# Kernel optimization log

Hardware: AMD Instinct MI355X
Metric: run time of the kernel (lower is better)

## Reference

```python
import jax, jax.numpy as jnp
import numpy as np

N = 50000      # num nodes
E = 800000     # num edges (no self loops; added in reference like add_remaining_self_loops)
D = 64         # input_dim
H = 128        # hidden_dim
O = 32         # output_dim
EPS = 1.0      # epsilon (privacy)
ALPHA = 0.5
DELTA = 1.0


def setup_inputs() -> dict:
    key = jax.random.key(0)
    ks = jax.random.split(key, 8)
    x = jax.random.normal(ks[0], (N, D), dtype=jnp.float32)
    row = jax.random.randint(ks[1], (E,), 0, N, dtype=jnp.int32)
    off = jax.random.randint(ks[2], (E,), 1, N, dtype=jnp.int32)
    col = (row + off) % N  # guarantees row != col (no pre-existing self loops)
    edge_index = jnp.stack([row, col], axis=0)
    priv_mask = jax.random.bernoulli(ks[3], 0.5, (N,))
    W1 = jax.random.normal(ks[4], (D, H), dtype=jnp.float32) * (1.0 / np.sqrt(D))
    b1 = jnp.zeros((H,), dtype=jnp.float32)
    W2 = jax.random.normal(ks[5], (H, O), dtype=jnp.float32) * (1.0 / np.sqrt(H))
    b2 = jnp.zeros((O,), dtype=jnp.float32)
    return {"x": x, "edge_index": edge_index, "priv_mask": priv_mask,
            "W1": W1, "b1": b1, "W2": W2, "b2": b2}


def _gcn_norm(edge_index, num_nodes, dtype):
    # add_remaining_self_loops + symmetric normalization deg^-1/2[row]*deg^-1/2[col]
    loops = jnp.arange(num_nodes, dtype=edge_index.dtype)
    row = jnp.concatenate([edge_index[0], loops])
    col = jnp.concatenate([edge_index[1], loops])
    deg = jax.ops.segment_sum(jnp.ones(row.shape[0], dtype=dtype), row,
                              num_segments=num_nodes)
    dis = deg ** -0.5  # deg >= 1 thanks to self loops
    norm = dis[row] * dis[col]  # [E+N]
    return row, col, norm


def reference(x, edge_index, priv_mask, W1, b1, W2, b2):
    row, col, norm = _gcn_norm(edge_index, N, x.dtype)
    exp_eps = float(np.exp(EPS))

    # ---- conv1 (GConvDP with per-node bool priv_mask) ----
    x_j = x[row]                                   # [E+N, D] gather
    p = priv_mask[row].astype(x.dtype)[:, None]    # [E+N, 1]
    transformed = ((exp_eps + 1.0) * x_j - 1.0) * (DELTA / (exp_eps - 1.0)) + ALPHA
    msg = norm[:, None] * (p * transformed + (1.0 - p) * x_j)
    h = jax.ops.segment_sum(msg, col, num_segments=N)  # scatter-add aggregate

    h = jax.nn.relu(h @ W1 + b1)
    # F.dropout skipped: reference is deterministic (eval mode)

    # ---- conv2 (called with priv_mask=False, a Python scalar) ----
    # Literal torch semantics: p_j = False -> False*(...) = 0, ~False = -1,
    # so msg = norm * (-x_j).
    msg2 = -norm[:, None] * h[row]                 # [E+N, H]
    h2 = jax.ops.segment_sum(msg2, col, num_segments=N)

    return h2 @ W2 + b2
```

## Files before the change

kernel.cpp:

```cpp
#include <hip/hip_runtime.h>
#include <math.h>

#define C1 2.163953413738653f
#define C0 -0.081976706869326f


typedef __attribute__((ext_vector_type(8))) short bf16x8;
typedef __attribute__((ext_vector_type(4))) float f32x4;

static __device__ __forceinline__ unsigned short f2bf(float f) {
    unsigned b = __float_as_uint(f);
    return (unsigned short)((b + 0x7FFFu + ((b >> 16) & 1u)) >> 16);
}
static __device__ __forceinline__ float bf2f(unsigned short u) {
    return __uint_as_float((unsigned)u << 16);
}
static __device__ __forceinline__ float bfl(unsigned u) { return __uint_as_float(u << 16); }
static __device__ __forceinline__ float bfh(unsigned u) { return __uint_as_float(u & 0xFFFF0000u); }

__global__ __launch_bounds__(1024) void k_hist2(const int* __restrict__ row,
                                                const int* __restrict__ col, int E, int chunk,
                                                int* __restrict__ hist,
                                                const float* __restrict__ W1,
                                                const float* __restrict__ W2,
                                                unsigned short* __restrict__ W1b,
                                                unsigned short* __restrict__ W2b) {
    __shared__ int hc[256], hr[256];
    int t = threadIdx.x, b = blockIdx.x;
    if (t < 256) { hc[t] = 0; hr[t] = 0; }
    __syncthreads();
    int lo = b * chunk, hi = min(E, lo + chunk);
    int base = lo + t * 4;
    for (; base + 3 < hi; base += 4096) {
        int4 r4 = *(const int4*)&row[base];
        int4 c4 = *(const int4*)&col[base];
        atomicAdd(&hc[c4.x >> 8], 1); atomicAdd(&hc[c4.y >> 8], 1);
        atomicAdd(&hc[c4.z >> 8], 1); atomicAdd(&hc[c4.w >> 8], 1);
        atomicAdd(&hr[r4.x >> 8], 1); atomicAdd(&hr[r4.y >> 8], 1);
        atomicAdd(&hr[r4.z >> 8], 1); atomicAdd(&hr[r4.w >> 8], 1);
    }
    for (; base < hi; ++base) {
        atomicAdd(&hc[col[base] >> 8], 1);
        atomicAdd(&hr[row[base] >> 8], 1);
    }
    __syncthreads();
    if (t < 256) {
        hist[t * 256 + b] = hc[t];
        hist[65536 + t * 256 + b] = hr[t];
    }
    if (b == 0) {
        for (int i = t; i < 8192; i += 1024) {
            int j = i & 7, l2 = (i >> 3) & 63, kt = (i >> 9) & 1, nt = i >> 10;
            int k = kt * 32 + (l2 >> 4) * 8 + j, n = nt * 16 + (l2 & 15);
            W1b[i] = f2bf(W1[k * 128 + n]);
        }
    } else if (b == 1) {
        for (int i = t; i < 4096; i += 1024) {
            int j = i & 7, l2 = (i >> 3) & 63, kt = (i >> 9) & 3, nt = i >> 11;
            int k = kt * 32 + (l2 >> 4) * 8 + j, n = nt * 16 + (l2 & 15);
            W2b[i] = f2bf(W2[k * 32 + n]);
        }
    }
}

__global__ void k_scan_a(const int* __restrict__ cnt, int* __restrict__ excl,
                         int* __restrict__ bsum, int n) {
    __shared__ int s[256];
    int idx = blockIdx.x * 256 + threadIdx.x;
    int v = (idx < n) ? cnt[idx] : 0;
    s[threadIdx.x] = v;
    __syncthreads();
    for (int off = 1; off < 256; off <<= 1) {
        int t = (threadIdx.x >= off) ? s[threadIdx.x - off] : 0;
        __syncthreads();
        s[threadIdx.x] += t;
        __syncthreads();
    }
    if (idx < n) excl[idx] = s[threadIdx.x] - v;
    if (threadIdx.x == 255) bsum[blockIdx.x] = s[255];
}

__global__ __launch_bounds__(1024) void k_part(const int* __restrict__ row,
                                               const int* __restrict__ col, int E, int chunk,
                                               const int* __restrict__ excl,
                                               const int* __restrict__ bsum,
                                               unsigned* __restrict__ cbuf,
                                               unsigned char* __restrict__ rbuf) {
    __shared__ int sc[512];
    __shared__ int offc[256], offr[256];
    int t = threadIdx.x, b = blockIdx.x;
    if (t < 512) sc[t] = bsum[t];
    __syncthreads();
    int half = t >> 8, d = t & 255;
    for (int off = 1; off < 256; off <<= 1) {
        int u = (t < 512 && d >= off) ? sc[half * 256 + d - off] : 0;
        __syncthreads();
        if (t < 512) sc[t] += u;
        __syncthreads();
    }
    if (t < 256) offc[t] = sc[t] - bsum[t] + excl[t * 256 + b];
    else if (t < 512) offr[d] = sc[t] - bsum[t] + excl[65536 + d * 256 + b];
    __syncthreads();
    int lo = b * chunk, hi = min(E, lo + chunk);
    int base = lo + t * 4;
    for (; base + 3 < hi; base += 4096) {
        int4 r4 = *(const int4*)&row[base];
        int4 c4 = *(const int4*)&col[base];
        int p0 = atomicAdd(&offc[c4.x >> 8], 1);
        cbuf[p0] = ((unsigned)c4.x << 16) | (unsigned)r4.x;
        int p1 = atomicAdd(&offc[c4.y >> 8], 1);
        cbuf[p1] = ((unsigned)c4.y << 16) | (unsigned)r4.y;
        int p2 = atomicAdd(&offc[c4.z >> 8], 1);
        cbuf[p2] = ((unsigned)c4.z << 16) | (unsigned)r4.z;
        int p3 = atomicAdd(&offc[c4.w >> 8], 1);
        cbuf[p3] = ((unsigned)c4.w << 16) | (unsigned)r4.w;
        int q0 = atomicAdd(&offr[r4.x >> 8], 1); rbuf[q0] = (unsigned char)r4.x;
        int q1 = atomicAdd(&offr[r4.y >> 8], 1); rbuf[q1] = (unsigned char)r4.y;
        int q2 = atomicAdd(&offr[r4.z >> 8], 1); rbuf[q2] = (unsigned char)r4.z;
        int q3 = atomicAdd(&offr[r4.w >> 8], 1); rbuf[q3] = (unsigned char)r4.w;
    }
    for (; base < hi; ++base) {
        int r = row[base], c = col[base];
        int pc = atomicAdd(&offc[c >> 8], 1);
        cbuf[pc] = ((unsigned)c << 16) | (unsigned)r;
        int pr = atomicAdd(&offr[r >> 8], 1);
        rbuf[pr] = (unsigned char)r;
    }
}

__global__ __launch_bounds__(256) void k_build(const unsigned char* __restrict__ rbuf,
                                               const unsigned* __restrict__ cbuf,
                                               const int* __restrict__ bsum,
                                               const int* __restrict__ priv,
                                               const float* __restrict__ x, int N, int E, int nbk,
                                               float* __restrict__ dis,
                                               unsigned short* __restrict__ xt,
                                               int* __restrict__ cntC, int* __restrict__ colStart,
                                               unsigned short* __restrict__ eSrc) {
    __shared__ int s1[256], s2[256], s3[256];
    int t = threadIdx.x;
    if ((int)blockIdx.x < nbk) {
        int b = blockIdx.x;
        s1[t] = (t < b) ? bsum[256 + t] : 0;
        __syncthreads();
        for (int off = 128; off > 0; off >>= 1) {
            if (t < off) s1[t] += s1[t + off];
            __syncthreads();
        }
        int rs = s1[0];
        int re = rs + bsum[256 + b];
        __syncthreads();
        s1[t] = 0;
        __syncthreads();
        for (int i = rs + t; i < re; i += 256) atomicAdd(&s1[rbuf[i]], 1);
        __syncthreads();
        int node = b * 256 + t;
        float dv = rsqrtf((float)(s1[t] + 1));
        if (node < N) {
            dis[node] = dv;
            s2[t] = __float_as_int(dv);
            s3[t] = priv[node];
        } else { s2[t] = 0; s3[t] = 0; }
        __syncthreads();
        int base = b * 256;
        for (int i = t; i < 256 * 16; i += 256) {
            int ln = i >> 4;
            int n2 = base + ln;
            if (n2 >= N) continue;
            float d2 = __int_as_float(s2[ln]);
            int p = s3[ln];
            float4 v = ((const float4*)x)[(size_t)n2 * 16 + (i & 15)];
            float4 tr;
            tr.x = p ? fmaf(C1, v.x, C0) : v.x;
            tr.y = p ? fmaf(C1, v.y, C0) : v.y;
            tr.z = p ? fmaf(C1, v.z, C0) : v.z;
            tr.w = p ? fmaf(C1, v.w, C0) : v.w;
            ushort4 o;
            o.x = f2bf(d2 * tr.x); o.y = f2bf(d2 * tr.y);
            o.z = f2bf(d2 * tr.z); o.w = f2bf(d2 * tr.w);
            ((ushort4*)xt)[(size_t)n2 * 16 + (i & 15)] = o;
        }
    } else {
        int b = blockIdx.x - nbk;
        s1[t] = (t < b) ? bsum[t] : 0;
        __syncthreads();
        for (int off = 128; off > 0; off >>= 1) {
            if (t < off) s1[t] += s1[t + off];
            __syncthreads();
        }
        int cs = s1[0];
        int ce = cs + bsum[b];
        __syncthreads();
        s1[t] = 0; s3[t] = 0;
        __syncthreads();
        for (int i = cs + t; i < ce; i += 256) atomicAdd(&s1[(cbuf[i] >> 16) & 255], 1);
        __syncthreads();
        int v = s1[t];
        s2[t] = v;
        __syncthreads();
        for (int off = 1; off < 256; off <<= 1) {
            int u = (t >= off) ? s2[t - off] : 0;
            __syncthreads();
            s2[t] += u;
            __syncthreads();
        }
        int excl = s2[t] - v;
        int c = b * 256 + t;
        if (c < N) { cntC[c] = v; colStart[c] = cs + excl; }
        __syncthreads();
        s2[t] = excl;
        __syncthreads();
        for (int i = cs + t; i < ce; i += 256) {
            unsigned e = cbuf[i];
            int d = (e >> 16) & 255;
            int pos = cs + s2[d] + atomicAdd(&s3[d], 1);
            eSrc[pos] = (unsigned short)(e & 0xFFFFu);
        }
    }
}

__global__ __launch_bounds__(256) void k_gather1(const unsigned short* __restrict__ xt,
                                                 const unsigned short* __restrict__ eSrc,
                                                 const int* __restrict__ colStart,
                                                 const int* __restrict__ cntC,
                                                 const float* __restrict__ dis,
                                                 unsigned short* __restrict__ agg1b, int N) {
    int t = blockIdx.x * blockDim.x + threadIdx.x;
    int c = t >> 4, j = t & 15;
    if (c >= N) return;
    const uint2* x64 = (const uint2*)xt;
    uint2 u = x64[(size_t)c * 16 + j];
    float s0 = bfl(u.x), s1 = bfh(u.x), s2 = bfl(u.y), s3 = bfh(u.y);
    int start = colStart[c], cnt = cntC[c];
    for (int base = 0; base < cnt; base += 16) {
        int m = min(cnt - base, 16);
        int ids = (j < m) ? (int)eSrc[start + base + j] : 0;
        int k = 0;
        for (; k + 8 <= m; k += 8) {
            int r0 = __shfl(ids, k, 16),     r1 = __shfl(ids, k + 1, 16);
            int r2 = __shfl(ids, k + 2, 16), r3 = __shfl(ids, k + 3, 16);
            int r4 = __shfl(ids, k + 4, 16), r5 = __shfl(ids, k + 5, 16);
            int r6 = __shfl(ids, k + 6, 16), r7 = __shfl(ids, k + 7, 16);
            uint2 u0 = x64[(size_t)r0 * 16 + j];
            uint2 u1 = x64[(size_t)r1 * 16 + j];
            uint2 u2 = x64[(size_t)r2 * 16 + j];
            uint2 u3 = x64[(size_t)r3 * 16 + j];
            uint2 u4 = x64[(size_t)r4 * 16 + j];
            uint2 u5 = x64[(size_t)r5 * 16 + j];
            uint2 u6 = x64[(size_t)r6 * 16 + j];
            uint2 u7 = x64[(size_t)r7 * 16 + j];
            s0 += bfl(u0.x); s1 += bfh(u0.x); s2 += bfl(u0.y); s3 += bfh(u0.y);
            s0 += bfl(u1.x); s1 += bfh(u1.x); s2 += bfl(u1.y); s3 += bfh(u1.y);
            s0 += bfl(u2.x); s1 += bfh(u2.x); s2 += bfl(u2.y); s3 += bfh(u2.y);
            s0 += bfl(u3.x); s1 += bfh(u3.x); s2 += bfl(u3.y); s3 += bfh(u3.y);
            s0 += bfl(u4.x); s1 += bfh(u4.x); s2 += bfl(u4.y); s3 += bfh(u4.y);
            s0 += bfl(u5.x); s1 += bfh(u5.x); s2 += bfl(u5.y); s3 += bfh(u5.y);
            s0 += bfl(u6.x); s1 += bfh(u6.x); s2 += bfl(u6.y); s3 += bfh(u6.y);
            s0 += bfl(u7.x); s1 += bfh(u7.x); s2 += bfl(u7.y); s3 += bfh(u7.y);
        }
        for (; k + 4 <= m; k += 4) {
            int r0 = __shfl(ids, k, 16),     r1 = __shfl(ids, k + 1, 16);
            int r2 = __shfl(ids, k + 2, 16), r3 = __shfl(ids, k + 3, 16);
            uint2 u0 = x64[(size_t)r0 * 16 + j];
            uint2 u1 = x64[(size_t)r1 * 16 + j];
            uint2 u2 = x64[(size_t)r2 * 16 + j];
            uint2 u3 = x64[(size_t)r3 * 16 + j];
            s0 += bfl(u0.x); s1 += bfh(u0.x); s2 += bfl(u0.y); s3 += bfh(u0.y);
            s0 += bfl(u1.x); s1 += bfh(u1.x); s2 += bfl(u1.y); s3 += bfh(u1.y);
            s0 += bfl(u2.x); s1 += bfh(u2.x); s2 += bfl(u2.y); s3 += bfh(u2.y);
            s0 += bfl(u3.x); s1 += bfh(u3.x); s2 += bfl(u3.y); s3 += bfh(u3.y);
        }
        for (; k < m; ++k) {
            int r = __shfl(ids, k, 16);
            uint2 uu = x64[(size_t)r * 16 + j];
            s0 += bfl(uu.x); s1 += bfh(uu.x); s2 += bfl(uu.y); s3 += bfh(uu.y);
        }
    }
    float dv = dis[c];
    uint2 o;
    o.x = ((unsigned)f2bf(dv * s1) << 16) | (unsigned)f2bf(dv * s0);
    o.y = ((unsigned)f2bf(dv * s3) << 16) | (unsigned)f2bf(dv * s2);
    ((uint2*)agg1b)[(size_t)c * 16 + j] = o;
}

__global__ __launch_bounds__(256) void k_mlp_mfma(const unsigned short* __restrict__ agg1b,
                                                  const unsigned short* __restrict__ W1b,
                                                  const float* __restrict__ b1,
                                                  const unsigned short* __restrict__ W2b,
                                                  const float* __restrict__ dis,
                                                  unsigned short* __restrict__ hps, int N) {
    __shared__ unsigned short hidA[4][16 * 136];
    const int t = threadIdx.x;
    const int w = t >> 6, l = t & 63;
    const int q = l >> 4, lm = l & 15;
    const int rowbase = blockIdx.x * 64 + w * 16;

    bf16x8 a0, a1;
    {
        int node = rowbase + lm;
        if (node >= N) node = N - 1;
        const bf16x8* pa = (const bf16x8*)(agg1b + (size_t)node * 64);
        a0 = pa[q];
        a1 = pa[4 + q];
    }
    float dvals[4];
    #pragma unroll
    for (int r = 0; r < 4; ++r) {
        int node = rowbase + q * 4 + r;
        dvals[r] = (node < N) ? dis[node] : 0.f;
    }

    const bf16x8* w1f = (const bf16x8*)W1b;
    #pragma unroll
    for (int nt = 0; nt < 8; ++nt) {
        float bv = b1[nt * 16 + lm];
        f32x4 acc = {bv, bv, bv, bv};
        acc = __builtin_amdgcn_mfma_f32_16x16x32_bf16(a0, w1f[(nt * 2 + 0) * 64 + l], acc, 0, 0, 0);
        acc = __builtin_amdgcn_mfma_f32_16x16x32_bf16(a1, w1f[(nt * 2 + 1) * 64 + l], acc, 0, 0, 0);
        #pragma unroll
        for (int r = 0; r < 4; ++r)
            hidA[w][(q * 4 + r) * 136 + nt * 16 + lm] = f2bf(fmaxf(acc[r], 0.f));
    }
    __syncthreads();

    bf16x8 ha[4];
    #pragma unroll
    for (int kt = 0; kt < 4; ++kt)
        ha[kt] = *(const bf16x8*)&hidA[w][lm * 136 + kt * 32 + q * 8];

    const bf16x8* w2f = (const bf16x8*)W2b;
    #pragma unroll
    for (int nt = 0; nt < 2; ++nt) {
        f32x4 acc = {0.f, 0.f, 0.f, 0.f};
        #pragma unroll
        for (int kt = 0; kt < 4; ++kt)
            acc = __builtin_amdgcn_mfma_f32_16x16x32_bf16(ha[kt], w2f[(nt * 4 + kt) * 64 + l], acc, 0, 0, 0);
        #pragma unroll
        for (int r = 0; r < 4; ++r) {
            int node = rowbase + q * 4 + r;
            if (node < N)
                hps[(size_t)node * 32 + nt * 16 + lm] = f2bf(acc[r] * dvals[r]);
        }
    }
}

__global__ __launch_bounds__(256) void k_gather2(const unsigned short* __restrict__ hps,
                                                 const unsigned short* __restrict__ eSrc,
                                                 const int* __restrict__ colStart,
                                                 const int* __restrict__ cntC,
                                                 const float* __restrict__ dis,
                                                 const float* __restrict__ b2,
                                                 float* __restrict__ out, int N) {
    int t = blockIdx.x * blockDim.x + threadIdx.x;
    int c = t >> 3, j = t & 7;
    if (c >= N) return;
    const uint2* h64 = (const uint2*)hps;
    uint2 u = h64[(size_t)c * 8 + j];
    float s0 = bfl(u.x), s1 = bfh(u.x), s2 = bfl(u.y), s3 = bfh(u.y);
    int start = colStart[c], cnt = cntC[c];
    for (int base = 0; base < cnt; base += 8) {
        int m = min(cnt - base, 8);
        int ids = (j < m) ? (int)eSrc[start + base + j] : 0;
        int k = 0;
        for (; k + 8 <= m; k += 8) {
            int r0 = __shfl(ids, k, 8),     r1 = __shfl(ids, k + 1, 8);
            int r2 = __shfl(ids, k + 2, 8), r3 = __shfl(ids, k + 3, 8);
            int r4 = __shfl(ids, k + 4, 8), r5 = __shfl(ids, k + 5, 8);
            int r6 = __shfl(ids, k + 6, 8), r7 = __shfl(ids, k + 7, 8);
            uint2 u0 = h64[(size_t)r0 * 8 + j];
            uint2 u1 = h64[(size_t)r1 * 8 + j];
            uint2 u2 = h64[(size_t)r2 * 8 + j];
            uint2 u3 = h64[(size_t)r3 * 8 + j];
            uint2 u4 = h64[(size_t)r4 * 8 + j];
            uint2 u5 = h64[(size_t)r5 * 8 + j];
            uint2 u6 = h64[(size_t)r6 * 8 + j];
            uint2 u7 = h64[(size_t)r7 * 8 + j];
            s0 += bfl(u0.x); s1 += bfh(u0.x); s2 += bfl(u0.y); s3 += bfh(u0.y);
            s0 += bfl(u1.x); s1 += bfh(u1.x); s2 += bfl(u1.y); s3 += bfh(u1.y);
            s0 += bfl(u2.x); s1 += bfh(u2.x); s2 += bfl(u2.y); s3 += bfh(u2.y);
            s0 += bfl(u3.x); s1 += bfh(u3.x); s2 += bfl(u3.y); s3 += bfh(u3.y);
            s0 += bfl(u4.x); s1 += bfh(u4.x); s2 += bfl(u4.y); s3 += bfh(u4.y);
            s0 += bfl(u5.x); s1 += bfh(u5.x); s2 += bfl(u5.y); s3 += bfh(u5.y);
            s0 += bfl(u6.x); s1 += bfh(u6.x); s2 += bfl(u6.y); s3 += bfh(u6.y);
            s0 += bfl(u7.x); s1 += bfh(u7.x); s2 += bfl(u7.y); s3 += bfh(u7.y);
        }
        for (; k + 4 <= m; k += 4) {
            int r0 = __shfl(ids, k, 8),     r1 = __shfl(ids, k + 1, 8);
            int r2 = __shfl(ids, k + 2, 8), r3 = __shfl(ids, k + 3, 8);
            uint2 u0 = h64[(size_t)r0 * 8 + j];
            uint2 u1 = h64[(size_t)r1 * 8 + j];
            uint2 u2 = h64[(size_t)r2 * 8 + j];
            uint2 u3 = h64[(size_t)r3 * 8 + j];
            s0 += bfl(u0.x); s1 += bfh(u0.x); s2 += bfl(u0.y); s3 += bfh(u0.y);
            s0 += bfl(u1.x); s1 += bfh(u1.x); s2 += bfl(u1.y); s3 += bfh(u1.y);
            s0 += bfl(u2.x); s1 += bfh(u2.x); s2 += bfl(u2.y); s3 += bfh(u2.y);
            s0 += bfl(u3.x); s1 += bfh(u3.x); s2 += bfl(u3.y); s3 += bfh(u3.y);
        }
        for (; k < m; ++k) {
            int r = __shfl(ids, k, 8);
            uint2 uu = h64[(size_t)r * 8 + j];
            s0 += bfl(uu.x); s1 += bfh(uu.x); s2 += bfl(uu.y); s3 += bfh(uu.y);
        }
    }
    float dv = dis[c];
    float4 bb = ((const float4*)b2)[j];
    float4 o;
    o.x = bb.x - dv * s0;
    o.y = bb.y - dv * s1;
    o.z = bb.z - dv * s2;
    o.w = bb.w - dv * s3;
    ((float4*)out)[(size_t)c * 8 + j] = o;
}

extern "C" void kernel_launch(void* const* d_in, const int* in_sizes, int n_in,
                              void* d_out, int out_size, void* d_ws, size_t ws_size,
                              hipStream_t stream) {
    const float* x    = (const float*)d_in[0];
    const int*   ei   = (const int*)d_in[1];
    const int*   priv = (const int*)d_in[2];
    const float* W1   = (const float*)d_in[3];
    const float* b1   = (const float*)d_in[4];
    const float* W2   = (const float*)d_in[5];
    const float* b2   = (const float*)d_in[6];
    float* out = (float*)d_out;

    const int N = in_sizes[2];
    const int E = in_sizes[1] / 2;
    const int* row = ei;
    const int* col = ei + E;

    char* ws = (char*)d_ws;
    size_t off = 0;
    auto take = [&](size_t bytes) { char* p = ws + off; off = (off + bytes + 255) & ~(size_t)255; return p; };
    int*            hist     = (int*)           take((size_t)131072 * 4);
    int*            excl     = (int*)           take((size_t)131072 * 4);
    int*            bsum     = (int*)           take(512 * 4);
    unsigned short* W1b      = (unsigned short*)take((size_t)8192 * 2);
    unsigned short* W2b      = (unsigned short*)take((size_t)4096 * 2);
    unsigned*       cbuf     = (unsigned*)      take((size_t)E * 4);
    unsigned char*  rbuf     = (unsigned char*) take((size_t)E);
    float*          dis      = (float*)         take((size_t)N * 4);
    int*            cntC     = (int*)           take((size_t)N * 4);
    int*            colStart = (int*)           take((size_t)N * 4);
    unsigned short* eSrc     = (unsigned short*)take((size_t)E * 2);
    unsigned short* xt       = (unsigned short*)take((size_t)N * 64 * 2);
    unsigned short* agg1b    = (unsigned short*)take((size_t)N * 64 * 2);
    unsigned short* hps      = (unsigned short*)take((size_t)N * 32 * 2);
    (void)ws_size;

    const int chunk = (((E + 255) / 256) + 3) & ~3;
    const int nbk = (N + 255) / 256;

    k_hist2   <<<256, 1024, 0, stream>>>(row, col, E, chunk, hist, W1, W2, W1b, W2b);
    k_scan_a  <<<512, 256, 0, stream>>>(hist, excl, bsum, 131072);
    k_part    <<<256, 1024, 0, stream>>>(row, col, E, chunk, excl, bsum, cbuf, rbuf);
    k_build   <<<2 * nbk, 256, 0, stream>>>(rbuf, cbuf, bsum, priv, x, N, E, nbk,
                                            dis, xt, cntC, colStart, eSrc);
    k_gather1 <<<((size_t)N * 16 + 255) / 256, 256, 0, stream>>>(xt, eSrc, colStart, cntC, dis, agg1b, N);
    k_mlp_mfma<<<(N + 63) / 64, 256, 0, stream>>>(agg1b, W1b, b1, W2b, dis, hps, N);
    k_gather2 <<<((size_t)N * 8 + 255) / 256, 256, 0, stream>>>(hps, eSrc, colStart, cntC, dis, b2, out, N);
}
```

Before: 145.2 us.

## Assign a full wavefront per node in both gather kernels with zero-padded sentinel rows

The two gather kernels now give each destination node a whole 64-lane wavefront instead of 16 or 8 lanes. Sub-groups of lanes fetch different neighbours at the same time and are combined with xor-shuffle reductions. Out-of-range neighbour slots point to a new zero row appended to xt and hps, which k_hist2 clears, so the tail loops need no per-lane branching. This raises memory-level parallelism for the average degree of about 16. The cost is four times more threads, idle lanes on low-degree nodes, and extra shuffle and reduction work.

```diff
diff --git a/kernel.cpp b/kernel.cpp
--- a/kernel.cpp
+++ b/kernel.cpp
@@ -24,7 +24,9 @@
                                                 const float* __restrict__ W1,
                                                 const float* __restrict__ W2,
                                                 unsigned short* __restrict__ W1b,
-                                                unsigned short* __restrict__ W2b) {
+                                                unsigned short* __restrict__ W2b,
+                                                unsigned short* __restrict__ xt,
+                                                unsigned short* __restrict__ hps, int N) {
     __shared__ int hc[256], hr[256];
     int t = threadIdx.x, b = blockIdx.x;
     if (t < 256) { hc[t] = 0; hr[t] = 0; }
@@ -60,6 +62,9 @@
             int k = kt * 32 + (l2 >> 4) * 8 + j, n = nt * 16 + (l2 & 15);
             W2b[i] = f2bf(W2[k * 32 + n]);
         }
+    } else if (b == 2) {
+        if (t < 64) xt[(size_t)N * 64 + t] = 0;
+        else if (t < 96) hps[(size_t)N * 32 + (t - 64)] = 0;
     }
 }
 
@@ -225,42 +230,23 @@
                                                  const int* __restrict__ cntC,
                                                  const float* __restrict__ dis,
                                                  unsigned short* __restrict__ agg1b, int N) {
-    int t = blockIdx.x * blockDim.x + threadIdx.x;
-    int c = t >> 4, j = t & 15;
+    int c = (blockIdx.x * blockDim.x + threadIdx.x) >> 6;
     if (c >= N) return;
+    int lane = threadIdx.x & 63;
+    int j = lane & 15;
+    int g = lane >> 4;
     const uint2* x64 = (const uint2*)xt;
-    uint2 u = x64[(size_t)c * 16 + j];
-    float s0 = bfl(u.x), s1 = bfh(u.x), s2 = bfl(u.y), s3 = bfh(u.y);
+    float s0 = 0.f, s1 = 0.f, s2 = 0.f, s3 = 0.f;
     int start = colStart[c], cnt = cntC[c];
-    for (int base = 0; base < cnt; base += 16) {
-        int m = min(cnt - base, 16);
-        int ids = (j < m) ? (int)eSrc[start + base + j] : 0;
+    for (int base = 0; base < cnt; base += 64) {
+        int m = min(cnt - base, 64);
+        int ids = (lane < m) ? (int)eSrc[start + base + lane] : N;
         int k = 0;
-        for (; k + 8 <= m; k += 8) {
-            int r0 = __shfl(ids, k, 16),     r1 = __shfl(ids, k + 1, 16);
-            int r2 = __shfl(ids, k + 2, 16), r3 = __shfl(ids, k + 3, 16);
-            int r4 = __shfl(ids, k + 4, 16), r5 = __shfl(ids, k + 5, 16);
-            int r6 = __shfl(ids, k + 6, 16), r7 = __shfl(ids, k + 7, 16);
-            uint2 u0 = x64[(size_t)r0 * 16 + j];
-            uint2 u1 = x64[(size_t)r1 * 16 + j];
-            uint2 u2 = x64[(size_t)r2 * 16 + j];
-            uint2 u3 = x64[(size_t)r3 * 16 + j];
-            uint2 u4 = x64[(size_t)r4 * 16 + j];
-            uint2 u5 = x64[(size_t)r5 * 16 + j];
-            uint2 u6 = x64[(size_t)r6 * 16 + j];
-            uint2 u7 = x64[(size_t)r7 * 16 + j];
-            s0 += bfl(u0.x); s1 += bfh(u0.x); s2 += bfl(u0.y); s3 += bfh(u0.y);
-            s0 += bfl(u1.x); s1 += bfh(u1.x); s2 += bfl(u1.y); s3 += bfh(u1.y);
-            s0 += bfl(u2.x); s1 += bfh(u2.x); s2 += bfl(u2.y); s3 += bfh(u2.y);
-            s0 += bfl(u3.x); s1 += bfh(u3.x); s2 += bfl(u3.y); s3 += bfh(u3.y);
-            s0 += bfl(u4.x); s1 += bfh(u4.x); s2 += bfl(u4.y); s3 += bfh(u4.y);
-            s0 += bfl(u5.x); s1 += bfh(u5.x); s2 += bfl(u5.y); s3 += bfh(u5.y);
-            s0 += bfl(u6.x); s1 += bfh(u6.x); s2 += bfl(u6.y); s3 += bfh(u6.y);
-            s0 += bfl(u7.x); s1 += bfh(u7.x); s2 += bfl(u7.y); s3 += bfh(u7.y);
-        }
-        for (; k + 4 <= m; k += 4) {
-            int r0 = __shfl(ids, k, 16),     r1 = __shfl(ids, k + 1, 16);
-            int r2 = __shfl(ids, k + 2, 16), r3 = __shfl(ids, k + 3, 16);
+        for (; k + 16 <= m; k += 16) {
+            int r0 = __shfl(ids, k + g, 64);
+            int r1 = __shfl(ids, k + 4 + g, 64);
+            int r2 = __shfl(ids, k + 8 + g, 64);
+            int r3 = __shfl(ids, k + 12 + g, 64);
             uint2 u0 = x64[(size_t)r0 * 16 + j];
             uint2 u1 = x64[(size_t)r1 * 16 + j];
             uint2 u2 = x64[(size_t)r2 * 16 + j];
@@ -270,17 +256,25 @@
             s0 += bfl(u2.x); s1 += bfh(u2.x); s2 += bfl(u2.y); s3 += bfh(u2.y);
             s0 += bfl(u3.x); s1 += bfh(u3.x); s2 += bfl(u3.y); s3 += bfh(u3.y);
         }
-        for (; k < m; ++k) {
-            int r = __shfl(ids, k, 16);
-            uint2 uu = x64[(size_t)r * 16 + j];
-            s0 += bfl(uu.x); s1 += bfh(uu.x); s2 += bfl(uu.y); s3 += bfh(uu.y);
-        }
-    }
-    float dv = dis[c];
-    uint2 o;
-    o.x = ((unsigned)f2bf(dv * s1) << 16) | (unsigned)f2bf(dv * s0);
-    o.y = ((unsigned)f2bf(dv * s3) << 16) | (unsigned)f2bf(dv * s2);
-    ((uint2*)agg1b)[(size_t)c * 16 + j] = o;
+        for (; k < m; k += 4) {
+            int r = __shfl(ids, k + g, 64);
+            uint2 u = x64[(size_t)r * 16 + j];
+            s0 += bfl(u.x); s1 += bfh(u.x); s2 += bfl(u.y); s3 += bfh(u.y);
+        }
+    }
+    s0 += __shfl_xor(s0, 32, 64); s1 += __shfl_xor(s1, 32, 64);
+    s2 += __shfl_xor(s2, 32, 64); s3 += __shfl_xor(s3, 32, 64);
+    s0 += __shfl_xor(s0, 16, 64); s1 += __shfl_xor(s1, 16, 64);
+    s2 += __shfl_xor(s2, 16, 64); s3 += __shfl_xor(s3, 16, 64);
+    if (g == 0) {
+        uint2 u = x64[(size_t)c * 16 + j];
+        s0 += bfl(u.x); s1 += bfh(u.x); s2 += bfl(u.y); s3 += bfh(u.y);
+        float dv = dis[c];
+        uint2 o;
+        o.x = ((unsigned)f2bf(dv * s1) << 16) | (unsigned)f2bf(dv * s0);
+        o.y = ((unsigned)f2bf(dv * s3) << 16) | (unsigned)f2bf(dv * s2);
+        ((uint2*)agg1b)[(size_t)c * 16 + j] = o;
+    }
 }
 
 __global__ __launch_bounds__(256) void k_mlp_mfma(const unsigned short* __restrict__ agg1b,
@@ -351,65 +345,50 @@
                                                  const float* __restrict__ dis,
                                                  const float* __restrict__ b2,
                                                  float* __restrict__ out, int N) {
-    int t = blockIdx.x * blockDim.x + threadIdx.x;
-    int c = t >> 3, j = t & 7;
+    int c = (blockIdx.x * blockDim.x + threadIdx.x) >> 6;
     if (c >= N) return;
+    int lane = threadIdx.x & 63;
+    int j = lane & 7;
+    int g = lane >> 3;
     const uint2* h64 = (const uint2*)hps;
-    uint2 u = h64[(size_t)c * 8 + j];
-    float s0 = bfl(u.x), s1 = bfh(u.x), s2 = bfl(u.y), s3 = bfh(u.y);
+    float s0 = 0.f, s1 = 0.f, s2 = 0.f, s3 = 0.f;
     int start = colStart[c], cnt = cntC[c];
-    for (int base = 0; base < cnt; base += 8) {
-        int m = min(cnt - base, 8);
-        int ids = (j < m) ? (int)eSrc[start + base + j] : 0;
+    for (int base = 0; base < cnt; base += 64) {
+        int m = min(cnt - base, 64);
+        int ids = (lane < m) ? (int)eSrc[start + base + lane] : N;
         int k = 0;
-        for (; k + 8 <= m; k += 8) {
-            int r0 = __shfl(ids, k, 8),     r1 = __shfl(ids, k + 1, 8);
-            int r2 = __shfl(ids, k + 2, 8), r3 = __shfl(ids, k + 3, 8);
-            int r4 = __shfl(ids, k + 4, 8), r5 = __shfl(ids, k + 5, 8);
-            int r6 = __shfl(ids, k + 6, 8), r7 = __shfl(ids, k + 7, 8);
+        for (; k + 16 <= m; k += 16) {
+            int r0 = __shfl(ids, k + g, 64);
+            int r1 = __shfl(ids, k + 8 + g, 64);
             uint2 u0 = h64[(size_t)r0 * 8 + j];
             uint2 u1 = h64[(size_t)r1 * 8 + j];
-            uint2 u2 = h64[(size_t)r2 * 8 + j];
-            uint2 u3 = h64[(size_t)r3 * 8 + j];
-            uint2 u4 = h64[(size_t)r4 * 8 + j];
-            uint2 u5 = h64[(size_t)r5 * 8 + j];
-            uint2 u6 = h64[(size_t)r6 * 8 + j];
-            uint2 u7 = h64[(size_t)r7 * 8 + j];
             s0 += bfl(u0.x); s1 += bfh(u0.x); s2 += bfl(u0.y); s3 += bfh(u0.y);
             s0 += bfl(u1.x); s1 += bfh(u1.x); s2 += bfl(u1.y); s3 += bfh(u1.y);
-            s0 += bfl(u2.x); s1 += bfh(u2.x); s2 += bfl(u2.y); s3 += bfh(u2.y);
-            s0 += bfl(u3.x); s1 += bfh(u3.x); s2 += bfl(u3.y); s3 += bfh(u3.y);
-            s0 += bfl(u4.x); s1 += bfh(u4.x); s2 += bfl(u4.y); s3 += bfh(u4.y);
-            s0 += bfl(u5.x); s1 += bfh(u5.x); s2 += bfl(u5.y); s3 += bfh(u5.y);
-            s0 += bfl(u6.x); s1 += bfh(u6.x); s2 += bfl(u6.y); s3 += bfh(u6.y);
-            s0 += bfl(u7.x); s1 += bfh(u7.x); s2 += bfl(u7.y); s3 += bfh(u7.y);
-        }
-        for (; k + 4 <= m; k += 4) {
-            int r0 = __shfl(ids, k, 8),     r1 = __shfl(ids, k + 1, 8);
-            int r2 = __shfl(ids, k + 2, 8), r3 = __shfl(ids, k + 3, 8);
-            uint2 u0 = h64[(size_t)r0 * 8 + j];
-            uint2 u1 = h64[(size_t)r1 * 8 + j];
-            uint2 u2 = h64[(size_t)r2 * 8 + j];
-            uint2 u3 = h64[(size_t)r3 * 8 + j];
-            s0 += bfl(u0.x); s1 += bfh(u0.x); s2 += bfl(u0.y); s3 += bfh(u0.y);
-            s0 += bfl(u1.x); s1 += bfh(u1.x); s2 += bfl(u1.y); s3 += bfh(u1.y);
-            s0 += bfl(u2.x); s1 += bfh(u2.x); s2 += bfl(u2.y); s3 += bfh(u2.y);
-            s0 += bfl(u3.x); s1 += bfh(u3.x); s2 += bfl(u3.y); s3 += bfh(u3.y);
-        }
-        for (; k < m; ++k) {
-            int r = __shfl(ids, k, 8);
-            uint2 uu = h64[(size_t)r * 8 + j];
-            s0 += bfl(uu.x); s1 += bfh(uu.x); s2 += bfl(uu.y); s3 += bfh(uu.y);
-        }
-    }
-    float dv = dis[c];
-    float4 bb = ((const float4*)b2)[j];
-    float4 o;
-    o.x = bb.x - dv * s0;
-    o.y = bb.y - dv * s1;
-    o.z = bb.z - dv * s2;
-    o.w = bb.w - dv * s3;
-    ((float4*)out)[(size_t)c * 8 + j] = o;
+        }
+        for (; k < m; k += 8) {
+            int r = __shfl(ids, k + g, 64);
+            uint2 u = h64[(size_t)r * 8 + j];
+            s0 += bfl(u.x); s1 += bfh(u.x); s2 += bfl(u.y); s3 += bfh(u.y);
+        }
+    }
+    s0 += __shfl_xor(s0, 32, 64); s1 += __shfl_xor(s1, 32, 64);
+    s2 += __shfl_xor(s2, 32, 64); s3 += __shfl_xor(s3, 32, 64);
+    s0 += __shfl_xor(s0, 16, 64); s1 += __shfl_xor(s1, 16, 64);
+    s2 += __shfl_xor(s2, 16, 64); s3 += __shfl_xor(s3, 16, 64);
+    s0 += __shfl_xor(s0, 8, 64);  s1 += __shfl_xor(s1, 8, 64);
+    s2 += __shfl_xor(s2, 8, 64);  s3 += __shfl_xor(s3, 8, 64);
+    if (g == 0) {
+        uint2 u = h64[(size_t)c * 8 + j];
+        s0 += bfl(u.x); s1 += bfh(u.x); s2 += bfl(u.y); s3 += bfh(u.y);
+        float dv = dis[c];
+        float4 bb = ((const float4*)b2)[j];
+        float4 o;
+        o.x = bb.x - dv * s0;
+        o.y = bb.y - dv * s1;
+        o.z = bb.z - dv * s2;
+        o.w = bb.w - dv * s3;
+        ((float4*)out)[(size_t)c * 8 + j] = o;
+    }
 }
 
 extern "C" void kernel_launch(void* const* d_in, const int* in_sizes, int n_in,
@@ -443,20 +422,20 @@
     int*            cntC     = (int*)           take((size_t)N * 4);
     int*            colStart = (int*)           take((size_t)N * 4);
     unsigned short* eSrc     = (unsigned short*)take((size_t)E * 2);
-    unsigned short* xt       = (unsigned short*)take((size_t)N * 64 * 2);
+    unsigned short* xt       = (unsigned short*)take((size_t)(N + 1) * 64 * 2);
     unsigned short* agg1b    = (unsigned short*)take((size_t)N * 64 * 2);
-    unsigned short* hps      = (unsigned short*)take((size_t)N * 32 * 2);
+    unsigned short* hps      = (unsigned short*)take((size_t)(N + 1) * 32 * 2);
     (void)ws_size;
 
     const int chunk = (((E + 255) / 256) + 3) & ~3;
     const int nbk = (N + 255) / 256;
 
-    k_hist2   <<<256, 1024, 0, stream>>>(row, col, E, chunk, hist, W1, W2, W1b, W2b);
+    k_hist2   <<<256, 1024, 0, stream>>>(row, col, E, chunk, hist, W1, W2, W1b, W2b, xt, hps, N);
     k_scan_a  <<<512, 256, 0, stream>>>(hist, excl, bsum, 131072);
     k_part    <<<256, 1024, 0, stream>>>(row, col, E, chunk, excl, bsum, cbuf, rbuf);
     k_build   <<<2 * nbk, 256, 0, stream>>>(rbuf, cbuf, bsum, priv, x, N, E, nbk,
                                             dis, xt, cntC, colStart, eSrc);
-    k_gather1 <<<((size_t)N * 16 + 255) / 256, 256, 0, stream>>>(xt, eSrc, colStart, cntC, dis, agg1b, N);
+    k_gather1 <<<((size_t)N * 64 + 255) / 256, 256, 0, stream>>>(xt, eSrc, colStart, cntC, dis, agg1b, N);
     k_mlp_mfma<<<(N + 63) / 64, 256, 0, stream>>>(agg1b, W1b, b1, W2b, dis, hps, N);
-    k_gather2 <<<((size_t)N * 8 + 255) / 256, 256, 0, stream>>>(hps, eSrc, colStart, cntC, dis, b2, out, N);
-}
+    k_gather2 <<<((size_t)N * 64 + 255) / 256, 256, 0, stream>>>(hps, eSrc, colStart, cntC, dis, b2, out, N);
+}
```

Result: slower. 159.2 us (+9.6%).

## Fuse first-layer gather into MLP kernel via shared-memory aggregate tile

Applied to the files above, without the earlier changes.

Merges the layer-1 neighbor gather with the MFMA MLP kernel. Each 256-thread block gathers 64 nodes (16 lanes per node, four passes) into a padded LDS tile, then runs the W1/W2 MFMA stages from LDS. This drops the agg1b global write and read-back and one kernel launch. In exchange the gather runs with fewer blocks, each doing four sequential node passes, which may reduce memory-level parallelism and latency hiding.

```diff
diff --git a/kernel.cpp b/kernel.cpp
--- a/kernel.cpp
+++ b/kernel.cpp
@@ -219,90 +219,87 @@
     }
 }
 
-__global__ __launch_bounds__(256) void k_gather1(const unsigned short* __restrict__ xt,
-                                                 const unsigned short* __restrict__ eSrc,
-                                                 const int* __restrict__ colStart,
-                                                 const int* __restrict__ cntC,
-                                                 const float* __restrict__ dis,
-                                                 unsigned short* __restrict__ agg1b, int N) {
-    int t = blockIdx.x * blockDim.x + threadIdx.x;
-    int c = t >> 4, j = t & 15;
-    if (c >= N) return;
-    const uint2* x64 = (const uint2*)xt;
-    uint2 u = x64[(size_t)c * 16 + j];
-    float s0 = bfl(u.x), s1 = bfh(u.x), s2 = bfl(u.y), s3 = bfh(u.y);
-    int start = colStart[c], cnt = cntC[c];
-    for (int base = 0; base < cnt; base += 16) {
-        int m = min(cnt - base, 16);
-        int ids = (j < m) ? (int)eSrc[start + base + j] : 0;
-        int k = 0;
-        for (; k + 8 <= m; k += 8) {
-            int r0 = __shfl(ids, k, 16),     r1 = __shfl(ids, k + 1, 16);
-            int r2 = __shfl(ids, k + 2, 16), r3 = __shfl(ids, k + 3, 16);
-            int r4 = __shfl(ids, k + 4, 16), r5 = __shfl(ids, k + 5, 16);
-            int r6 = __shfl(ids, k + 6, 16), r7 = __shfl(ids, k + 7, 16);
-            uint2 u0 = x64[(size_t)r0 * 16 + j];
-            uint2 u1 = x64[(size_t)r1 * 16 + j];
-            uint2 u2 = x64[(size_t)r2 * 16 + j];
-            uint2 u3 = x64[(size_t)r3 * 16 + j];
-            uint2 u4 = x64[(size_t)r4 * 16 + j];
-            uint2 u5 = x64[(size_t)r5 * 16 + j];
-            uint2 u6 = x64[(size_t)r6 * 16 + j];
-            uint2 u7 = x64[(size_t)r7 * 16 + j];
-            s0 += bfl(u0.x); s1 += bfh(u0.x); s2 += bfl(u0.y); s3 += bfh(u0.y);
-            s0 += bfl(u1.x); s1 += bfh(u1.x); s2 += bfl(u1.y); s3 += bfh(u1.y);
-            s0 += bfl(u2.x); s1 += bfh(u2.x); s2 += bfl(u2.y); s3 += bfh(u2.y);
-            s0 += bfl(u3.x); s1 += bfh(u3.x); s2 += bfl(u3.y); s3 += bfh(u3.y);
-            s0 += bfl(u4.x); s1 += bfh(u4.x); s2 += bfl(u4.y); s3 += bfh(u4.y);
-            s0 += bfl(u5.x); s1 += bfh(u5.x); s2 += bfl(u5.y); s3 += bfh(u5.y);
-            s0 += bfl(u6.x); s1 += bfh(u6.x); s2 += bfl(u6.y); s3 += bfh(u6.y);
-            s0 += bfl(u7.x); s1 += bfh(u7.x); s2 += bfl(u7.y); s3 += bfh(u7.y);
-        }
-        for (; k + 4 <= m; k += 4) {
-            int r0 = __shfl(ids, k, 16),     r1 = __shfl(ids, k + 1, 16);
-            int r2 = __shfl(ids, k + 2, 16), r3 = __shfl(ids, k + 3, 16);
-            uint2 u0 = x64[(size_t)r0 * 16 + j];
-            uint2 u1 = x64[(size_t)r1 * 16 + j];
-            uint2 u2 = x64[(size_t)r2 * 16 + j];
-            uint2 u3 = x64[(size_t)r3 * 16 + j];
-            s0 += bfl(u0.x); s1 += bfh(u0.x); s2 += bfl(u0.y); s3 += bfh(u0.y);
-            s0 += bfl(u1.x); s1 += bfh(u1.x); s2 += bfl(u1.y); s3 += bfh(u1.y);
-            s0 += bfl(u2.x); s1 += bfh(u2.x); s2 += bfl(u2.y); s3 += bfh(u2.y);
-            s0 += bfl(u3.x); s1 += bfh(u3.x); s2 += bfl(u3.y); s3 += bfh(u3.y);
-        }
-        for (; k < m; ++k) {
-            int r = __shfl(ids, k, 16);
-            uint2 uu = x64[(size_t)r * 16 + j];
-            s0 += bfl(uu.x); s1 += bfh(uu.x); s2 += bfl(uu.y); s3 += bfh(uu.y);
-        }
-    }
-    float dv = dis[c];
-    uint2 o;
-    o.x = ((unsigned)f2bf(dv * s1) << 16) | (unsigned)f2bf(dv * s0);
-    o.y = ((unsigned)f2bf(dv * s3) << 16) | (unsigned)f2bf(dv * s2);
-    ((uint2*)agg1b)[(size_t)c * 16 + j] = o;
-}
-
-__global__ __launch_bounds__(256) void k_mlp_mfma(const unsigned short* __restrict__ agg1b,
-                                                  const unsigned short* __restrict__ W1b,
-                                                  const float* __restrict__ b1,
-                                                  const unsigned short* __restrict__ W2b,
-                                                  const float* __restrict__ dis,
-                                                  unsigned short* __restrict__ hps, int N) {
+__global__ __launch_bounds__(256) void k_gmlp(const unsigned short* __restrict__ xt,
+                                              const unsigned short* __restrict__ eSrc,
+                                              const int* __restrict__ colStart,
+                                              const int* __restrict__ cntC,
+                                              const float* __restrict__ dis,
+                                              const unsigned short* __restrict__ W1b,
+                                              const float* __restrict__ b1,
+                                              const unsigned short* __restrict__ W2b,
+                                              unsigned short* __restrict__ hps, int N) {
+    __shared__ unsigned short agg[64 * 72];
     __shared__ unsigned short hidA[4][16 * 136];
     const int t = threadIdx.x;
+    const int grp = t >> 4, j = t & 15;
+    const uint2* x64 = (const uint2*)xt;
+
+    for (int it = 0; it < 4; ++it) {
+        int ln = grp + it * 16;
+        int c = blockIdx.x * 64 + ln;
+        uint2 o; o.x = 0u; o.y = 0u;
+        if (c < N) {
+            uint2 u = x64[(size_t)c * 16 + j];
+            float s0 = bfl(u.x), s1 = bfh(u.x), s2 = bfl(u.y), s3 = bfh(u.y);
+            int start = colStart[c], cnt = cntC[c];
+            for (int base = 0; base < cnt; base += 16) {
+                int m = min(cnt - base, 16);
+                int ids = (j < m) ? (int)eSrc[start + base + j] : 0;
+                int k = 0;
+                for (; k + 8 <= m; k += 8) {
+                    int r0 = __shfl(ids, k, 16),     r1 = __shfl(ids, k + 1, 16);
+                    int r2 = __shfl(ids, k + 2, 16), r3 = __shfl(ids, k + 3, 16);
+                    int r4 = __shfl(ids, k + 4, 16), r5 = __shfl(ids, k + 5, 16);
+                    int r6 = __shfl(ids, k + 6, 16), r7 = __shfl(ids, k + 7, 16);
+                    uint2 u0 = x64[(size_t)r0 * 16 + j];
+                    uint2 u1 = x64[(size_t)r1 * 16 + j];
+                    uint2 u2 = x64[(size_t)r2 * 16 + j];
+                    uint2 u3 = x64[(size_t)r3 * 16 + j];
+                    uint2 u4 = x64[(size_t)r4 * 16 + j];
+                    uint2 u5 = x64[(size_t)r5 * 16 + j];
+                    uint2 u6 = x64[(size_t)r6 * 16 + j];
+                    uint2 u7 = x64[(size_t)r7 * 16 + j];
+                    s0 += bfl(u0.x); s1 += bfh(u0.x); s2 += bfl(u0.y); s3 += bfh(u0.y);
+                    s0 += bfl(u1.x); s1 += bfh(u1.x); s2 += bfl(u1.y); s3 += bfh(u1.y);
+                    s0 += bfl(u2.x); s1 += bfh(u2.x); s2 += bfl(u2.y); s3 += bfh(u2.y);
+                    s0 += bfl(u3.x); s1 += bfh(u3.x); s2 += bfl(u3.y); s3 += bfh(u3.y);
+                    s0 += bfl(u4.x); s1 += bfh(u4.x); s2 += bfl(u4.y); s3 += bfh(u4.y);
+                    s0 += bfl(u5.x); s1 += bfh(u5.x); s2 += bfl(u5.y); s3 += bfh(u5.y);
+                    s0 += bfl(u6.x); s1 += bfh(u6.x); s2 += bfl(u6.y); s3 += bfh(u6.y);
+                    s0 += bfl(u7.x); s1 += bfh(u7.x); s2 += bfl(u7.y); s3 += bfh(u7.y);
+                }
+                for (; k + 4 <= m; k += 4) {
+                    int r0 = __shfl(ids, k, 16),     r1 = __shfl(ids, k + 1, 16);
+                    int r2 = __shfl(ids, k + 2, 16), r3 = __shfl(ids, k + 3, 16);
+                    uint2 u0 = x64[(size_t)r0 * 16 + j];
+                    uint2 u1 = x64[(size_t)r1 * 16 + j];
+                    uint2 u2 = x64[(size_t)r2 * 16 + j];
+                    uint2 u3 = x64[(size_t)r3 * 16 + j];
+                    s0 += bfl(u0.x); s1 += bfh(u0.x); s2 += bfl(u0.y); s3 += bfh(u0.y);
+                    s0 += bfl(u1.x); s1 += bfh(u1.x); s2 += bfl(u1.y); s3 += bfh(u1.y);
+                    s0 += bfl(u2.x); s1 += bfh(u2.x); s2 += bfl(u2.y); s3 += bfh(u2.y);
+                    s0 += bfl(u3.x); s1 += bfh(u3.x); s2 += bfl(u3.y); s3 += bfh(u3.y);
+                }
+                for (; k < m; ++k) {
+                    int r = __shfl(ids, k, 16);
+                    uint2 uu = x64[(size_t)r * 16 + j];
+                    s0 += bfl(uu.x); s1 += bfh(uu.x); s2 += bfl(uu.y); s3 += bfh(uu.y);
+                }
+            }
+            float dv = dis[c];
+            o.x = ((unsigned)f2bf(dv * s1) << 16) | (unsigned)f2bf(dv * s0);
+            o.y = ((unsigned)f2bf(dv * s3) << 16) | (unsigned)f2bf(dv * s2);
+        }
+        *(uint2*)&agg[ln * 72 + j * 4] = o;
+    }
+    __syncthreads();
+
     const int w = t >> 6, l = t & 63;
     const int q = l >> 4, lm = l & 15;
     const int rowbase = blockIdx.x * 64 + w * 16;
 
-    bf16x8 a0, a1;
-    {
-        int node = rowbase + lm;
-        if (node >= N) node = N - 1;
-        const bf16x8* pa = (const bf16x8*)(agg1b + (size_t)node * 64);
-        a0 = pa[q];
-        a1 = pa[4 + q];
-    }
+    bf16x8 a0 = *(const bf16x8*)&agg[(w * 16 + lm) * 72 + q * 8];
+    bf16x8 a1 = *(const bf16x8*)&agg[(w * 16 + lm) * 72 + 32 + q * 8];
     float dvals[4];
     #pragma unroll
     for (int r = 0; r < 4; ++r) {
@@ -444,7 +441,6 @@
     int*            colStart = (int*)           take((size_t)N * 4);
     unsigned short* eSrc     = (unsigned short*)take((size_t)E * 2);
     unsigned short* xt       = (unsigned short*)take((size_t)N * 64 * 2);
-    unsigned short* agg1b    = (unsigned short*)take((size_t)N * 64 * 2);
     unsigned short* hps      = (unsigned short*)take((size_t)N * 32 * 2);
     (void)ws_size;
 
@@ -456,7 +452,7 @@
     k_part    <<<256, 1024, 0, stream>>>(row, col, E, chunk, excl, bsum, cbuf, rbuf);
     k_build   <<<2 * nbk, 256, 0, stream>>>(rbuf, cbuf, bsum, priv, x, N, E, nbk,
                                             dis, xt, cntC, colStart, eSrc);
-    k_gather1 <<<((size_t)N * 16 + 255) / 256, 256, 0, stream>>>(xt, eSrc, colStart, cntC, dis, agg1b, N);
-    k_mlp_mfma<<<(N + 63) / 64, 256, 0, stream>>>(agg1b, W1b, b1, W2b, dis, hps, N);
+    k_gmlp    <<<(N + 63) / 64, 256, 0, stream>>>(xt, eSrc, colStart, cntC, dis,
+                                                  W1b, b1, W2b, hps, N);
     k_gather2 <<<((size_t)N * 8 + 255) / 256, 256, 0, stream>>>(hps, eSrc, colStart, cntC, dis, b2, out, N);
 }
```

Measured after the change: 151.1 us. +4.1%, slower.
